# Kernel tuning notes

Hardware: AMD Instinct MI355X
Metric: run time of the kernel (lower is better)

Reference implementation:

```python
import jax, jax.numpy as jnp
import numpy as np

N = 8192
E = 262144
DIN = 512
DOUT = 256


def setup_inputs() -> dict:
    key = jax.random.key(0)
    k1, k2, k3, k4 = jax.random.split(key, 4)
    x = jax.random.normal(k1, (N, DIN), dtype=jnp.float32)
    edge_index = jax.random.randint(k2, (2, E), 0, N, dtype=jnp.int64)
    edge_weight = jax.random.uniform(k3, (E,), dtype=jnp.float32)
    W = jax.random.normal(k4, (DOUT, DIN), dtype=jnp.float32) * (1.0 / np.sqrt(DIN))
    return {"x": x, "edge_index": edge_index, "edge_weight": edge_weight, "W": W}


def reference(x, edge_index, edge_weight, W):
    n = x.shape[0]
    # Linear(dim_in, dim_out, bias=False): h = x @ W.T  -> [N, DOUT]
    h = x @ W.T
    # Dense adjacency: A[src, dst] += w (to_dense_adj sums duplicate edges)
    src, dst = edge_index[0], edge_index[1]
    A = jnp.zeros((n, n), dtype=x.dtype).at[src, dst].add(edge_weight)
    # degree from A BEFORE self-loops, then +1 from the added eye on degree_matrix
    deg = jnp.sum(A, axis=1) + 1.0
    # sqrt(inverse(diag(deg))) == diag(1/sqrt(deg)); apply as row scaling
    dinv_sqrt = 1.0 / jnp.sqrt(deg)  # [N]
    A = A + jnp.eye(n, dtype=x.dtype)  # self-loops on adjacency
    # x = D^{-1/2} @ (A.T @ (D^{-1/2} @ h))
    h = dinv_sqrt[:, None] * h
    h = A.T @ h
    h = dinv_sqrt[:, None] * h
    return h
```

## Files before the change

### kernel.cpp

```cpp
#include <hip/hip_runtime.h>

static constexpr int DIN = 512;
static constexpr int DOUT = 256;
static constexpr int CAP = 128;
static constexpr int EPT = 8;

typedef __attribute__((ext_vector_type(8))) short short8;
typedef __attribute__((ext_vector_type(4))) float f32x4;
typedef __attribute__((ext_vector_type(2))) unsigned int u32x2;
typedef __attribute__((ext_vector_type(4))) unsigned int u32x4;

__device__ inline unsigned short f2bf(float f) {
  unsigned int b = __float_as_uint(f);
  unsigned int r = (b + 0x7fffu + ((b >> 16) & 1u)) >> 16;
  return (unsigned short)r;
}
__device__ inline float bf_lo(unsigned int packed) { return __uint_as_float(packed << 16); }
__device__ inline float bf_hi(unsigned int packed) { return __uint_as_float(packed & 0xffff0000u); }

__device__ inline short8 cvt8(const f32x4 a, const f32x4 b) {
  short8 o;
  o[0] = (short)f2bf(a[0]); o[1] = (short)f2bf(a[1]);
  o[2] = (short)f2bf(a[2]); o[3] = (short)f2bf(a[3]);
  o[4] = (short)f2bf(b[0]); o[5] = (short)f2bf(b[1]);
  o[6] = (short)f2bf(b[2]); o[7] = (short)f2bf(b[3]);
  return o;
}

__global__ __launch_bounds__(256) void k_prep(
    const float* __restrict__ W, unsigned short* __restrict__ wbb,
    int* __restrict__ dz, int n2, int wgroups) {
  const int gid = blockIdx.x * 256 + threadIdx.x;
  if (gid < n2) dz[gid] = 0;
  const int wi = gid - n2;
  if (wi >= 0 && wi < wgroups) {
    const f32x4* src = (const f32x4*)(W + (size_t)wi * 8);
    f32x4 a = src[0], b = src[1];
    *(short8*)(wbb + (size_t)wi * 8) = cvt8(a, b);
  }
}

__global__ __launch_bounds__(256) void k_work(
    const int* __restrict__ ei, const float* __restrict__ ew,
    const float* __restrict__ x, const unsigned short* __restrict__ wbb,
    float* __restrict__ deg, int* __restrict__ cursor,
    uint2* __restrict__ bucket, unsigned short* __restrict__ h1b,
    int E, int EBLK) {
  const int b = blockIdx.x;
  if (b < EBLK) {
    const int e0 = b * 256 * EPT + threadIdx.x;
    int sv[EPT], dv[EPT];
    float wv[EPT];
#pragma unroll
    for (int u = 0; u < EPT; ++u) {
      const int e = e0 + u * 256;
      sv[u] = __builtin_nontemporal_load(ei + e);
      dv[u] = __builtin_nontemporal_load(ei + E + e);
      wv[u] = __builtin_nontemporal_load(ew + e);
    }
    int pos[EPT];
#pragma unroll
    for (int u = 0; u < EPT; ++u) pos[u] = atomicAdd(&cursor[dv[u]], 1);
#pragma unroll
    for (int u = 0; u < EPT; ++u) atomicAdd(&deg[sv[u]], wv[u]);
#pragma unroll
    for (int u = 0; u < EPT; ++u) {
      if (pos[u] < CAP) {
        uint2 v;
        v.x = (unsigned)sv[u];
        v.y = __float_as_uint(wv[u]);
        bucket[(size_t)dv[u] * CAP + pos[u]] = v;
      }
    }
    return;
  }
  const int g = b - EBLK;
  const int lane = threadIdx.x & 63;
  const int wv = threadIdx.x >> 6;
  const int bm = g * 16;
  const int colb = wv * 64;
  const int r = lane & 15;
  const int kg = lane >> 4;
  f32x4 acc[4] = {};
  const float* arow = x + (size_t)(bm + r) * DIN + kg * 8;
  const unsigned short* brow0 = wbb + (size_t)(colb + r) * DIN + kg * 8;
#pragma unroll
  for (int k0 = 0; k0 < DIN; k0 += 32) {
    f32x4 a0 = *(const f32x4*)(arow + k0);
    f32x4 a1 = *(const f32x4*)(arow + k0 + 4);
    short8 av = cvt8(a0, a1);
#pragma unroll
    for (int nt = 0; nt < 4; ++nt) {
      short8 bv = *(const short8*)(brow0 + (size_t)nt * 16 * DIN + k0);
      acc[nt] = __builtin_amdgcn_mfma_f32_16x16x32_bf16(av, bv, acc[nt], 0, 0, 0);
    }
  }
#pragma unroll
  for (int i = 0; i < 4; ++i) {
    int row = bm + kg * 4 + i;
#pragma unroll
    for (int nt = 0; nt < 4; ++nt) {
      h1b[(size_t)row * DOUT + colb + nt * 16 + r] = f2bf(acc[nt][i]);
    }
  }
}

__global__ __launch_bounds__(256, 4) void k_gather(
    const unsigned short* __restrict__ h1b, const float* __restrict__ deg,
    const int* __restrict__ cursor, const uint2* __restrict__ bucket,
    float* __restrict__ out) {
  const int lane = threadIdx.x & 63;
  const int wv = threadIdx.x >> 6;
  const int dst = blockIdx.x * 4 + wv;
  const int cl = lane & 31;
  const int half = lane >> 5;
  const int cnt = min(cursor[dst], CAP);

  const u32x4 selfv = *(const u32x4*)(h1b + (size_t)dst * DOUT + cl * 8);
  const float sd = __frsqrt_rn(1.0f + deg[dst]);

  float acc[8] = {};

  for (int base = 0; base < cnt; base += 64) {
    const int c = min(64, cnt - base);
    int sv = 0;
    float wl = 0.f;
    if (lane < c) {
      u32x2 ev = __builtin_nontemporal_load(
          (const u32x2*)(bucket + (size_t)dst * CAP + base + lane));
      sv = (int)ev[0];
      wl = __uint_as_float(ev[1]) * __frsqrt_rn(1.0f + deg[sv]);
    }
    const int npair = ((c + 15) >> 4) << 3;
    for (int j = 0; j < npair; j += 8) {
      u32x4 rbuf[8];
#pragma unroll
      for (int u = 0; u < 8; ++u) {
        int src = __shfl(sv, 2 * (j + u) + half);
        rbuf[u] = *(const u32x4*)(h1b + (size_t)src * DOUT + cl * 8);
      }
#pragma unroll
      for (int u = 0; u < 8; ++u) {
        float w = __shfl(wl, 2 * (j + u) + half);
        acc[0] = fmaf(w, bf_lo(rbuf[u][0]), acc[0]);
        acc[1] = fmaf(w, bf_hi(rbuf[u][0]), acc[1]);
        acc[2] = fmaf(w, bf_lo(rbuf[u][1]), acc[2]);
        acc[3] = fmaf(w, bf_hi(rbuf[u][1]), acc[3]);
        acc[4] = fmaf(w, bf_lo(rbuf[u][2]), acc[4]);
        acc[5] = fmaf(w, bf_hi(rbuf[u][2]), acc[5]);
        acc[6] = fmaf(w, bf_lo(rbuf[u][3]), acc[6]);
        acc[7] = fmaf(w, bf_hi(rbuf[u][3]), acc[7]);
      }
    }
  }

#pragma unroll
  for (int k = 0; k < 8; ++k) acc[k] += __shfl_xor(acc[k], 32);

  if (half == 0) {
    f32x4 o0v, o1v;
    o0v[0] = sd * fmaf(sd, bf_lo(selfv[0]), acc[0]);
    o0v[1] = sd * fmaf(sd, bf_hi(selfv[0]), acc[1]);
    o0v[2] = sd * fmaf(sd, bf_lo(selfv[1]), acc[2]);
    o0v[3] = sd * fmaf(sd, bf_hi(selfv[1]), acc[3]);
    o1v[0] = sd * fmaf(sd, bf_lo(selfv[2]), acc[4]);
    o1v[1] = sd * fmaf(sd, bf_hi(selfv[2]), acc[5]);
    o1v[2] = sd * fmaf(sd, bf_lo(selfv[3]), acc[6]);
    o1v[3] = sd * fmaf(sd, bf_hi(selfv[3]), acc[7]);
    float* op = out + (size_t)dst * DOUT + cl * 8;
    __builtin_nontemporal_store(o0v, (f32x4*)op);
    __builtin_nontemporal_store(o1v, (f32x4*)(op + 4));
  }
}

extern "C" void kernel_launch(void* const* d_in, const int* in_sizes, int n_in,
                              void* d_out, int out_size, void* d_ws, size_t ws_size,
                              hipStream_t stream) {
  const float* x = (const float*)d_in[0];
  const int* ei = (const int*)d_in[1];
  const float* ew = (const float*)d_in[2];
  const float* W = (const float*)d_in[3];
  float* out = (float*)d_out;

  const int n = in_sizes[0] / DIN;
  const int E = in_sizes[2];

  char* p = (char*)d_ws;
  auto alloc = [&](size_t bytes) {
    char* q = p;
    p += (bytes + 255) & ~(size_t)255;
    return q;
  };
  unsigned short* h1b = (unsigned short*)alloc((size_t)n * DOUT * 2);
  unsigned short* wbb = (unsigned short*)alloc((size_t)DOUT * DIN * 2);
  float* deg   = (float*)alloc((size_t)n * 4 * 2);
  int* cursor  = (int*)(deg + n);
  uint2* bucket = (uint2*)alloc((size_t)n * CAP * 8);

  const int n2 = 2 * n;
  const int wgroups = DOUT * DIN / 8;
  const int prep_blocks = (n2 + wgroups + 255) / 256;

  const int EBLK = E / (256 * EPT);
  const int GB = n / 16;

  k_prep<<<prep_blocks, 256, 0, stream>>>(W, wbb, (int*)deg, n2, wgroups);
  k_work<<<EBLK + GB, 256, 0, stream>>>(ei, ew, x, wbb, deg, cursor, bucket,
                                        h1b, E, EBLK);
  k_gather<<<n / 4, 256, 0, stream>>>(h1b, deg, cursor, bucket, out);
}
```

Baseline: 70.78 us.

## Split fused edge/GEMM kernel and switch degree accumulation to fixed-point int atomics

```diff
diff --git a/kernel.cpp b/kernel.cpp
--- a/kernel.cpp
+++ b/kernel.cpp
@@ -4,6 +4,8 @@
 static constexpr int DOUT = 256;
 static constexpr int CAP = 128;
 static constexpr int EPT = 8;
+static constexpr float DEG_SCALE = 1048576.0f;
+static constexpr float DEG_INV = 1.0f / 1048576.0f;
 
 typedef __attribute__((ext_vector_type(8))) short short8;
 typedef __attribute__((ext_vector_type(4))) float f32x4;
@@ -40,44 +42,44 @@
   }
 }
 
-__global__ __launch_bounds__(256) void k_work(
+__global__ __launch_bounds__(256) void k_deg(
     const int* __restrict__ ei, const float* __restrict__ ew,
+    int* __restrict__ degi, int E) {
+  const int e0 = blockIdx.x * 256 * EPT + threadIdx.x;
+  int sv[EPT], wq[EPT];
+#pragma unroll
+  for (int u = 0; u < EPT; ++u) {
+    const int e = e0 + u * 256;
+    sv[u] = __builtin_nontemporal_load(ei + e);
+    wq[u] = __float2int_rn(__builtin_nontemporal_load(ew + e) * DEG_SCALE);
+  }
+#pragma unroll
+  for (int u = 0; u < EPT; ++u) atomicAdd(&degi[sv[u]], wq[u]);
+}
+
+__global__ __launch_bounds__(256) void k_bin(
+    const int* __restrict__ ei, const float* __restrict__ ew,
+    int* __restrict__ cursor, uint2* __restrict__ bucket, int E) {
+  const int e = blockIdx.x * 256 + threadIdx.x;
+  if (e >= E) return;
+  int srcv = __builtin_nontemporal_load(ei + e);
+  int dstv = __builtin_nontemporal_load(ei + E + e);
+  float w = __builtin_nontemporal_load(ew + e);
+  int pos = atomicAdd(&cursor[dstv], 1);
+  if (pos < CAP) {
+    u32x2 v;
+    v[0] = (unsigned)srcv;
+    v[1] = __float_as_uint(w);
+    __builtin_nontemporal_store(v, (u32x2*)(bucket + (size_t)dstv * CAP + pos));
+  }
+}
+
+__global__ __launch_bounds__(256) void k_gemm(
     const float* __restrict__ x, const unsigned short* __restrict__ wbb,
-    float* __restrict__ deg, int* __restrict__ cursor,
-    uint2* __restrict__ bucket, unsigned short* __restrict__ h1b,
-    int E, int EBLK) {
-  const int b = blockIdx.x;
-  if (b < EBLK) {
-    const int e0 = b * 256 * EPT + threadIdx.x;
-    int sv[EPT], dv[EPT];
-    float wv[EPT];
-#pragma unroll
-    for (int u = 0; u < EPT; ++u) {
-      const int e = e0 + u * 256;
-      sv[u] = __builtin_nontemporal_load(ei + e);
-      dv[u] = __builtin_nontemporal_load(ei + E + e);
-      wv[u] = __builtin_nontemporal_load(ew + e);
-    }
-    int pos[EPT];
-#pragma unroll
-    for (int u = 0; u < EPT; ++u) pos[u] = atomicAdd(&cursor[dv[u]], 1);
-#pragma unroll
-    for (int u = 0; u < EPT; ++u) atomicAdd(&deg[sv[u]], wv[u]);
-#pragma unroll
-    for (int u = 0; u < EPT; ++u) {
-      if (pos[u] < CAP) {
-        uint2 v;
-        v.x = (unsigned)sv[u];
-        v.y = __float_as_uint(wv[u]);
-        bucket[(size_t)dv[u] * CAP + pos[u]] = v;
-      }
-    }
-    return;
-  }
-  const int g = b - EBLK;
+    unsigned short* __restrict__ h1b) {
   const int lane = threadIdx.x & 63;
   const int wv = threadIdx.x >> 6;
-  const int bm = g * 16;
+  const int bm = blockIdx.x * 16;
   const int colb = wv * 64;
   const int r = lane & 15;
   const int kg = lane >> 4;
@@ -106,7 +108,7 @@
 }
 
 __global__ __launch_bounds__(256, 4) void k_gather(
-    const unsigned short* __restrict__ h1b, const float* __restrict__ deg,
+    const unsigned short* __restrict__ h1b, const int* __restrict__ degi,
     const int* __restrict__ cursor, const uint2* __restrict__ bucket,
     float* __restrict__ out) {
   const int lane = threadIdx.x & 63;
@@ -117,7 +119,7 @@
   const int cnt = min(cursor[dst], CAP);
 
   const u32x4 selfv = *(const u32x4*)(h1b + (size_t)dst * DOUT + cl * 8);
-  const float sd = __frsqrt_rn(1.0f + deg[dst]);
+  const float sd = __frsqrt_rn(1.0f + (float)degi[dst] * DEG_INV);
 
   float acc[8] = {};
 
@@ -129,7 +131,8 @@
       u32x2 ev = __builtin_nontemporal_load(
           (const u32x2*)(bucket + (size_t)dst * CAP + base + lane));
       sv = (int)ev[0];
-      wl = __uint_as_float(ev[1]) * __frsqrt_rn(1.0f + deg[sv]);
+      wl = __uint_as_float(ev[1]) *
+           __frsqrt_rn(1.0f + (float)degi[sv] * DEG_INV);
     }
     const int npair = ((c + 15) >> 4) << 3;
     for (int j = 0; j < npair; j += 8) {
@@ -193,19 +196,17 @@
   };
   unsigned short* h1b = (unsigned short*)alloc((size_t)n * DOUT * 2);
   unsigned short* wbb = (unsigned short*)alloc((size_t)DOUT * DIN * 2);
-  float* deg   = (float*)alloc((size_t)n * 4 * 2);
-  int* cursor  = (int*)(deg + n);
+  int* degi    = (int*)alloc((size_t)n * 4 * 2);
+  int* cursor  = degi + n;
   uint2* bucket = (uint2*)alloc((size_t)n * CAP * 8);
 
   const int n2 = 2 * n;
   const int wgroups = DOUT * DIN / 8;
   const int prep_blocks = (n2 + wgroups + 255) / 256;
 
-  const int EBLK = E / (256 * EPT);
-  const int GB = n / 16;
-
-  k_prep<<<prep_blocks, 256, 0, stream>>>(W, wbb, (int*)deg, n2, wgroups);
-  k_work<<<EBLK + GB, 256, 0, stream>>>(ei, ew, x, wbb, deg, cursor, bucket,
-                                        h1b, E, EBLK);
-  k_gather<<<n / 4, 256, 0, stream>>>(h1b, deg, cursor, bucket, out);
-}
+  k_prep<<<prep_blocks, 256, 0, stream>>>(W, wbb, degi, n2, wgroups);
+  k_deg<<<E / (256 * EPT), 256, 0, stream>>>(ei, ew, degi, E);
+  k_bin<<<(E + 255) / 256, 256, 0, stream>>>(ei, ew, cursor, bucket, E);
+  k_gemm<<<n / 16, 256, 0, stream>>>(x, wbb, h1b);
+  k_gather<<<n / 4, 256, 0, stream>>>(h1b, degi, cursor, bucket, out);
+}
```

Measured after the change: 81.01 us. 14.5% more time.
